# Optimization experiments

Measured on AMD Instinct MI355X. Metric: run time of the kernel, lower is better.

Reference implementation:

```python
import jax, jax.numpy as jnp
import numpy as np

B, T_TEXT, HID = 16, 512, 512
MAX_LEN = 2048
DP_CH, DP_K = 256, 3
PP_CH, PP_K, PP_LAYERS = 384, 5, 5
N_BINS = 256


def conv1d_same(x, w, b, pad):
    # x: [B, C_in, T], w: [C_out, C_in, K] -> [B, C_out, T]
    xp = jnp.pad(x, ((0, 0), (0, 0), (pad, pad)))
    y = jax.lax.conv_general_dilated(xp, w, (1,), 'VALID',
                                     dimension_numbers=('NCH', 'OIH', 'NCH'))
    return y + b[None, :, None]


def channel_ln(x, g, beta, eps=1e-5):
    # LayerNorm over channel dim of [B, C, T] (torch LayerNorm with dim=1)
    m = jnp.mean(x, axis=1, keepdims=True)
    v = jnp.mean((x - m) ** 2, axis=1, keepdims=True)
    return (x - m) / jnp.sqrt(v + eps) * g[None, :, None] + beta[None, :, None]


def sinusoidal_pos(T, dim):
    # fairseq-style sinusoidal embedding, positions start at padding_idx+1 = 1
    half = dim // 2
    inv = jnp.exp(jnp.arange(half, dtype=jnp.float32) * (-np.log(10000.0) / (half - 1)))
    pos = jnp.arange(1, T + 1, dtype=jnp.float32)
    ang = pos[:, None] * inv[None, :]
    return jnp.concatenate([jnp.sin(ang), jnp.cos(ang)], axis=1)  # [T, dim]


def setup_inputs() -> dict:
    key = jax.random.key(0)
    ks = jax.random.split(key, 16)
    sd = lambda fan: 1.0 / np.sqrt(fan)
    inp = {}
    inp['x'] = jax.random.normal(ks[0], (B, T_TEXT, HID), dtype=jnp.float32)
    inp['duration'] = jax.random.randint(ks[1], (B, T_TEXT), 0, 7, dtype=jnp.int32)
    inp['src_mask'] = jnp.zeros((B, T_TEXT), dtype=bool)
    inp['max_len'] = MAX_LEN
    # duration predictor params (2 conv layers + linear)
    inp['dp_w0'] = jax.random.normal(ks[2], (DP_CH, HID, DP_K)) * sd(HID * DP_K)
    inp['dp_w1'] = jax.random.normal(ks[3], (DP_CH, DP_CH, DP_K)) * sd(DP_CH * DP_K)
    inp['dp_b'] = jnp.zeros((2, DP_CH))
    inp['dp_g'] = jnp.ones((2, DP_CH))
    inp['dp_beta'] = jnp.zeros((2, DP_CH))
    inp['dp_lin_w'] = jax.random.normal(ks[4], (DP_CH, 1)) * sd(DP_CH)
    inp['dp_lin_b'] = jnp.zeros((1,))
    # pitch predictor params (5 conv layers + linear, odim=2 for use_uv)
    inp['pp_w0'] = jax.random.normal(ks[5], (PP_CH, HID, PP_K)) * sd(HID * PP_K)
    inp['pp_w_rest'] = jax.random.normal(ks[6], (PP_LAYERS - 1, PP_CH, PP_CH, PP_K)) * sd(PP_CH * PP_K)
    inp['pp_b'] = jnp.zeros((PP_LAYERS, PP_CH))
    inp['pp_g'] = jnp.ones((PP_LAYERS, PP_CH))
    inp['pp_beta'] = jnp.zeros((PP_LAYERS, PP_CH))
    inp['pp_lin_w'] = jax.random.normal(ks[7], (PP_CH, 2)) * sd(PP_CH)
    inp['pp_lin_b'] = jnp.zeros((2,))
    inp['pos_alpha'] = jnp.ones((1,))
    inp['pitch_emb'] = jax.random.normal(ks[8], (N_BINS, HID)) * 0.02
    inp['pitch_bins'] = jnp.linspace(-1.0, 1.0, N_BINS - 1)  # linear quantization, stats min/max
    return inp


def reference(x, duration, src_mask, max_len, dp_w0, dp_w1, dp_b, dp_g, dp_beta,
              dp_lin_w, dp_lin_b, pp_w0, pp_w_rest, pp_b, pp_g, pp_beta,
              pp_lin_w, pp_lin_b, pos_alpha, pitch_emb, pitch_bins):
    Bn, T, H = x.shape
    keep = 1.0 - src_mask.astype(x.dtype)  # [B,T], 1 where valid

    # ---- DurationPredictor (log-domain durations) ----
    h = jnp.transpose(x, (0, 2, 1))  # [B,H,T]
    for i, w in enumerate([dp_w0, dp_w1]):
        h = conv1d_same(h, w, dp_b[i], (DP_K - 1) // 2)
        h = jax.nn.relu(h)
        h = channel_ln(h, dp_g[i], dp_beta[i])
        h = h * keep[:, None, :]
    log_dur = (jnp.einsum('bct,co->bto', h, dp_lin_w) + dp_lin_b) * keep[:, :, None]
    log_dur = log_dur[..., 0]  # [B,T]

    # ---- LengthRegulator: vectorized variable-repeat via searchsorted ----
    cum = jnp.cumsum(duration, axis=1)  # [B,T]
    frames = jnp.arange(max_len)
    tok = jax.vmap(lambda c: jnp.searchsorted(c, frames, side='right'))(cum)  # [B,max_len]
    mel_len = cum[:, -1]
    fmask = (frames[None, :] < mel_len[:, None]).astype(x.dtype)  # [B,max_len]
    mel = jnp.take_along_axis(x, jnp.minimum(tok, T - 1)[..., None], axis=1) * fmask[..., None]

    # ---- VariancePredictor (pitch, odim=2 for f0 + uv) ----
    pe = sinusoidal_pos(max_len, H)  # [max_len, H]
    p = mel + pos_alpha[0] * pe[None]
    p = jnp.transpose(p, (0, 2, 1))  # [B,H,max_len]
    for i in range(PP_LAYERS):
        w = pp_w0 if i == 0 else pp_w_rest[i - 1]
        p = conv1d_same(p, w, pp_b[i], (PP_K - 1) // 2)
        p = jax.nn.relu(p)
        p = channel_ln(p, pp_g[i], pp_beta[i])
    pitch_pred = jnp.einsum('bct,co->bto', p, pp_lin_w) + pp_lin_b  # [B,max_len,2]

    # ---- bucketize f0 channel + embedding add ----
    idx = jnp.searchsorted(pitch_bins, pitch_pred[..., 0], side='left')  # torch.bucketize
    p_embed = pitch_emb[idx]  # [B,max_len,H]
    out = mel + p_embed
    return out, log_dur, pitch_pred, mel_len
```

## Files before the change

kernel.cpp:

```cpp
#include <hip/hip_runtime.h>
#include <cstdint>
#include <cstddef>

constexpr int BB      = 16;
constexpr int T_TEXT  = 512;
constexpr int HID     = 512;
constexpr int MAX_LEN = 2048;
constexpr int DP_CH   = 256;
constexpr int PP_CH   = 384;

typedef unsigned short u16;
typedef unsigned int   u32;
typedef short bf16x8 __attribute__((ext_vector_type(8)));
typedef float f32x4  __attribute__((ext_vector_type(4)));
typedef float f32x16 __attribute__((ext_vector_type(16)));

__device__ __forceinline__ void gload_lds16(const void* g, void* l) {
  __builtin_amdgcn_global_load_lds(
      (const __attribute__((address_space(1))) u32*)g,
      (__attribute__((address_space(3))) u32*)l, 16, 0, 0);
}

template <int N> __device__ __forceinline__ void vm_wait() {
  if constexpr (N == 0)      asm volatile("s_waitcnt vmcnt(0)" ::: "memory");
  else if constexpr (N == 3) asm volatile("s_waitcnt vmcnt(3)" ::: "memory");
  else if constexpr (N == 5) asm volatile("s_waitcnt vmcnt(5)" ::: "memory");
  else static_assert(N == 0, "unsupported vmcnt literal");
}

__device__ __forceinline__ u16 f2bf(float v) {
  union { float f; u32 u; } a;
  a.f = v;
  u32 r = (a.u + 0x7FFFu + ((a.u >> 16) & 1u)) >> 16;
  return (u16)r;
}
__device__ __forceinline__ float bf2f(u16 h) {
  union { u32 u; float f; } a;
  a.u = (u32)h << 16;
  return a.f;
}

__global__ __launch_bounds__(256) void pack_w_k(const float* __restrict__ w,
                                                u16* __restrict__ p,
                                                int O, int I, int KT) {
  int NF  = O >> 4, NCB = I >> 5;
  int total = KT * NCB * NF * 64;
  int idx = blockIdx.x * 256 + threadIdx.x;
  if (idx >= total) return;
  int l  = idx & 63;
  int f  = (idx >> 6) % NF;
  int cb = ((idx >> 6) / NF) % NCB;
  int k  = (idx >> 6) / (NF * NCB);
  int o  = f * 16 + (l & 15);
  int ib = cb * 32 + (l >> 4) * 8;
  u16* pd = p + ((size_t)((k * NCB + cb) * NF + f)) * 512 + (size_t)l * 8;
#pragma unroll
  for (int j = 0; j < 8; ++j)
    pd[j] = f2bf(w[((size_t)o * I + ib + j) * KT + k]);
}

__global__ __launch_bounds__(256) void pack_w32_k(const float* __restrict__ w,
                                                  u16* __restrict__ p,
                                                  int O, int I, int KT) {
  int G = O >> 5, NCB = I >> 5;
  int total = KT * NCB * G * 2 * 64;
  int idx = blockIdx.x * 256 + threadIdx.x;
  if (idx >= total) return;
  int l  = idx & 63;
  int ks = (idx >> 6) & 1;
  int g  = (idx >> 7) % G;
  int cb = ((idx >> 7) / G) % NCB;
  int k  = (idx >> 7) / (G * NCB);
  int o  = g * 32 + (l & 31);
  int ib = cb * 32 + ks * 16 + (l >> 5) * 8;
  u16* pd = p + (size_t)idx * 8;
#pragma unroll
  for (int j = 0; j < 8; ++j)
    pd[j] = f2bf(w[((size_t)o * I + ib + j) * KT + k]);
}

template <int CIN, int COUT, int KT, int MT, int WM, int WN, int OPAD, bool F32OUT>
__global__ __launch_bounds__(WM * WN * 64)
void gemm_conv_ln(const u16* __restrict__ a, const u16* __restrict__ wp,
                  const float* __restrict__ bias, const float* __restrict__ gamma,
                  const float* __restrict__ beta,
                  u16* __restrict__ o, float* __restrict__ fo, int T) {
  constexpr int WAVES   = WM * WN;
  constexpr int THREADS = WAVES * 64;
  constexpr int RS    = MT + KT - 1;
  constexpr int NCB   = CIN / 32;
  constexpr int NF    = COUT / 16;
  constexpr int Mfr   = MT / (16 * WM);
  constexpr int Nfr   = NF / WN;
  constexpr int A_ONE = RS * 64;
  constexpr int B_ONE = NF * 1024;
  constexpr int B_OFF = 2 * A_ONE;
  constexpr int RED_OFF = B_OFF + 2 * B_ONE;
  constexpr int CPW = 4 * RS / WAVES;

  const int TpIn  = T + KT - 1;
  const int TpOut = T + 2 * OPAD;

  const int tid  = threadIdx.x;
  const int wave = tid >> 6;
  const int lane = tid & 63;
  const int sl   = lane & 15;
  const int q    = lane >> 4;
  const int wm   = wave / WN;
  const int wn   = wave % WN;
  const int waveM0 = wm * Mfr * 16;
  const int f0   = wn * Nfr;
  const int t0   = blockIdx.x * MT;
  const int b    = blockIdx.y;

  extern __shared__ __align__(16) char smem[];
  const u16* abase_g = a + ((size_t)b * TpIn + t0) * CIN;

  auto stageA = [&](int buf, int cb) {
    char* lbase = smem + buf * A_ONE;
#pragma unroll
    for (int j = 0; j < CPW; j += 64) {
      int c   = wave * CPW + j + lane;
      int qc  = c / RS;
      int row = c - qc * RS;
      if (j + lane < CPW)
        gload_lds16(abase_g + (size_t)row * CIN + cb * 32 + qc * 8,
                    lbase + (size_t)(wave * CPW + j) * 16);
    }
  };
  auto stageB = [&](int buf, int k, int cb) {
    const u16* src = wp + ((size_t)(k * NCB + cb) * NF) * 512;
    char* lbase = smem + B_OFF + buf * B_ONE;
#pragma unroll
    for (int i = tid; i < NF * 64; i += THREADS) {
      gload_lds16(src + (size_t)i * 8, lbase + (size_t)(i - lane) * 16);
    }
  };

  f32x4 acc[Mfr][Nfr];
#pragma unroll
  for (int mf = 0; mf < Mfr; ++mf)
#pragma unroll
    for (int nf = 0; nf < Nfr; ++nf) acc[mf][nf] = (f32x4)0.f;

  stageA(0, 0);
  stageB(0, 0, 0);
  asm volatile("s_waitcnt vmcnt(0)" ::: "memory");
  __syncthreads();
  int ab = 0, bb = 0;
  for (int cb = 0; cb < NCB; ++cb) {
    for (int k = 0; k < KT; ++k) {
      if (k + 1 < KT) {
        stageB(bb ^ 1, k + 1, cb);
      } else if (cb + 1 < NCB) {
        stageB(bb ^ 1, 0, cb + 1);
        stageA(ab ^ 1, cb + 1);
      }
      bf16x8 A[Mfr], Bf[Nfr];
      const char* ab_l = smem + ab * A_ONE;
#pragma unroll
      for (int mf = 0; mf < Mfr; ++mf) {
        int row = waveM0 + mf * 16 + sl + k;
        A[mf] = *(const bf16x8*)(ab_l + (q * RS + row) * 16);
      }
      const char* bb_l = smem + B_OFF + bb * B_ONE;
#pragma unroll
      for (int nf = 0; nf < Nfr; ++nf)
        Bf[nf] = *(const bf16x8*)(bb_l + (size_t)(f0 + nf) * 1024 + lane * 16);
#pragma unroll
      for (int nf = 0; nf < Nfr; ++nf)
#pragma unroll
        for (int mf = 0; mf < Mfr; ++mf)
          acc[mf][nf] = __builtin_amdgcn_mfma_f32_16x16x32_bf16(
              A[mf], Bf[nf], acc[mf][nf], 0, 0, 0);
      asm volatile("s_waitcnt vmcnt(0)" ::: "memory");
      __syncthreads();
      bb ^= 1;
      if (k == KT - 1) ab ^= 1;
    }
  }

  float bc[Nfr], gc[Nfr], btc[Nfr];
#pragma unroll
  for (int nf = 0; nf < Nfr; ++nf) {
    int col = (f0 + nf) * 16 + sl;
    bc[nf]  = bias[col];
    gc[nf]  = gamma[col];
    btc[nf] = beta[col];
  }

  float* reds  = (float*)(smem + RED_OFF);
  float* redss = reds + MT * WN;

#pragma unroll
  for (int mf = 0; mf < Mfr; ++mf) {
#pragma unroll
    for (int r = 0; r < 4; ++r) {
      float s = 0.f, ss2 = 0.f;
#pragma unroll
      for (int nf = 0; nf < Nfr; ++nf) {
        float x = acc[mf][nf][r] + bc[nf];
        x = fmaxf(x, 0.f);
        acc[mf][nf][r] = x;
        s += x;
        ss2 = fmaf(x, x, ss2);
      }
#pragma unroll
      for (int off = 1; off < 16; off <<= 1) {
        s   += __shfl_xor(s, off, 64);
        ss2 += __shfl_xor(ss2, off, 64);
      }
      if (sl == 0) {
        int rowb = waveM0 + mf * 16 + q * 4 + r;
        reds[rowb * WN + wn]  = s;
        redss[rowb * WN + wn] = ss2;
      }
    }
  }
  __syncthreads();

#pragma unroll
  for (int mf = 0; mf < Mfr; ++mf) {
#pragma unroll
    for (int r = 0; r < 4; ++r) {
      int rowb = waveM0 + mf * 16 + q * 4 + r;
      float s = 0.f, ss2 = 0.f;
#pragma unroll
      for (int w2 = 0; w2 < WN; ++w2) {
        s   += reds[rowb * WN + w2];
        ss2 += redss[rowb * WN + w2];
      }
      float mean = s * (1.f / COUT);
      float var  = ss2 * (1.f / COUT) - mean * mean;
      float rstd = 1.f / sqrtf(var + 1e-5f);
      int trow = t0 + rowb;
#pragma unroll
      for (int nf = 0; nf < Nfr; ++nf) {
        int col = (f0 + nf) * 16 + sl;
        float y = (acc[mf][nf][r] - mean) * rstd * gc[nf] + btc[nf];
        if constexpr (F32OUT) {
          fo[((size_t)b * T + trow) * COUT + col] = y;
        } else {
          o[((size_t)b * TpOut + OPAD + trow) * COUT + col] = f2bf(y);
        }
      }
    }
  }

  if constexpr (!F32OUT && OPAD > 0) {
    if (blockIdx.x == 0) {
      for (int i = tid; i < OPAD * COUT; i += THREADS) {
        o[(size_t)b * TpOut * COUT + i] = 0;
        o[((size_t)b * TpOut + OPAD + T) * COUT + i] = 0;
      }
    }
  }
}

constexpr int gemm_lds(int MT, int KT, int COUT, int WN_) {
  return 2 * (MT + KT - 1) * 64 + 2 * (COUT / 16) * 1024 + MT * WN_ * 8;
}

template <int CIN, int COUT, int KT, int MT, int WM, int WN, int OPAD>
__global__ __launch_bounds__(WM * WN * 64)
void gemm_conv_ln32(const u16* __restrict__ a, const u16* __restrict__ wp,
                    const float* __restrict__ bias, const float* __restrict__ gamma,
                    const float* __restrict__ beta,
                    u16* __restrict__ o, int T) {
  constexpr int WAVES   = WM * WN;
  constexpr int THREADS = WAVES * 64;
  constexpr int RS    = MT + KT - 1;
  constexpr int NCB   = CIN / 32;
  constexpr int G     = COUT / 32;
  constexpr int Mfr   = MT / (32 * WM);
  constexpr int Nfr   = G / WN;
  constexpr int A_ONE = RS * 64;
  constexpr int NFB   = G * 2;
  constexpr int B_ONE = NFB * 1024;
  constexpr int B_OFF = 2 * A_ONE;
  constexpr int RED_OFF = B_OFF + KT * B_ONE;
  constexpr int NSTEPS = NCB * KT;
  static_assert((4 * RS) % WAVES == 0, "A chunks split evenly per wave");
  static_assert((NFB * 64) % THREADS == 0, "B chunks split evenly");
  constexpr int CPW = 4 * RS / WAVES;

  const int TpIn  = T + KT - 1;
  const int TpOut = T + 2 * OPAD;

  const int tid  = threadIdx.x;
  const int wave = tid >> 6;
  const int lane = tid & 63;
  const int l31  = lane & 31;
  const int lh   = lane >> 5;
  const int wm   = wave / WN;
  const int wn   = wave % WN;
  const int waveM0 = wm * Mfr * 32;
  const int g0   = wn * Nfr;
  const int t0   = blockIdx.x * MT;
  const int b    = blockIdx.y;

  extern __shared__ __align__(16) char smem[];
  const u16* abase_g = a + ((size_t)b * TpIn + t0) * CIN;

  auto stageA = [&](int buf, int cb) {
    char* lbase = smem + buf * A_ONE;
#pragma unroll
    for (int j = 0; j < CPW; j += 64) {
      int c   = wave * CPW + j + lane;
      int qc  = c / RS;
      int row = c - qc * RS;
      if (j + lane < CPW)
        gload_lds16(abase_g + (size_t)row * CIN + cb * 32 + qc * 8,
                    lbase + (size_t)(wave * CPW + j) * 16);
    }
  };
  auto stageB = [&](int buf, int k, int cb) {
    const u16* src = wp + ((size_t)(k * NCB + cb) * NFB) * 512;
    char* lbase = smem + B_OFF + buf * B_ONE;
#pragma unroll
    for (int i = tid; i < NFB * 64; i += THREADS) {
      gload_lds16(src + (size_t)i * 8, lbase + (size_t)(i - lane) * 16);
    }
  };

  f32x16 acc[Mfr][Nfr];
#pragma unroll
  for (int mf = 0; mf < Mfr; ++mf)
#pragma unroll
    for (int nf = 0; nf < Nfr; ++nf) acc[mf][nf] = (f32x16)0.f;

  stageA(0, 0);
  stageB(0, 0, 0);
  stageB(1, 1, 0);
  vm_wait<3>();
  __builtin_amdgcn_s_barrier();

  for (int cb = 0; cb < NCB; ++cb) {
    const char* ab_l = smem + (cb & 1) * A_ONE;
#pragma unroll
    for (int j = 0; j < KT; ++j) {
      const int s = cb * KT + j;
      __builtin_amdgcn_sched_barrier(0);

      bf16x8 A[Mfr][2], Bf[Nfr][2];
      const char* bb_l = smem + B_OFF + j * B_ONE;
#pragma unroll
      for (int mf = 0; mf < Mfr; ++mf) {
        int row = waveM0 + mf * 32 + l31 + j;
#pragma unroll
        for (int ks = 0; ks < 2; ++ks)
          A[mf][ks] = *(const bf16x8*)(ab_l + ((ks * 2 + lh) * RS + row) * 16);
      }
#pragma unroll
      for (int nf = 0; nf < Nfr; ++nf)
#pragma unroll
        for (int ks = 0; ks < 2; ++ks)
          Bf[nf][ks] = *(const bf16x8*)(bb_l + ((size_t)((g0 + nf) * 2 + ks)) * 1024 + lane * 16);

      const bool boundary = (j == 0 && cb + 1 < NCB);
      if (boundary) stageA((cb + 1) & 1, cb + 1);
      if (s + 2 < NSTEPS) {
        const int s2 = s + 2;
        stageB(s2 % KT, s2 % KT, s2 / KT);
      }

      __builtin_amdgcn_s_setprio(1);
#pragma unroll
      for (int ks = 0; ks < 2; ++ks)
#pragma unroll
        for (int nf = 0; nf < Nfr; ++nf)
#pragma unroll
          for (int mf = 0; mf < Mfr; ++mf)
            acc[mf][nf] = __builtin_amdgcn_mfma_f32_32x32x16_bf16(
                A[mf][ks], Bf[nf][ks], acc[mf][nf], 0, 0, 0);
      __builtin_amdgcn_s_setprio(0);

      __builtin_amdgcn_sched_barrier(0);
      if (s + 2 < NSTEPS) {
        if (boundary) vm_wait<5>();
        else          vm_wait<3>();
      } else {
        vm_wait<0>();
      }
      __builtin_amdgcn_s_barrier();
    }
  }

  float bc[Nfr], gc[Nfr], btc[Nfr];
#pragma unroll
  for (int nf = 0; nf < Nfr; ++nf) {
    int col = (g0 + nf) * 32 + l31;
    bc[nf]  = bias[col];
    gc[nf]  = gamma[col];
    btc[nf] = beta[col];
  }

  float* reds  = (float*)(smem + RED_OFF);
  float* redss = reds + MT * WN;
  float* mrs   = redss + MT * WN;

#pragma unroll
  for (int mf = 0; mf < Mfr; ++mf) {
#pragma unroll
    for (int r = 0; r < 16; ++r) {
      float s = 0.f, ss2 = 0.f;
#pragma unroll
      for (int nf = 0; nf < Nfr; ++nf) {
        float x = acc[mf][nf][r] + bc[nf];
        x = fmaxf(x, 0.f);
        acc[mf][nf][r] = x;
        s += x;
        ss2 = fmaf(x, x, ss2);
      }
#pragma unroll
      for (int off = 1; off < 32; off <<= 1) {
        s   += __shfl_xor(s, off, 64);
        ss2 += __shfl_xor(ss2, off, 64);
      }
      if (l31 == 0) {
        int row = waveM0 + mf * 32 + (r & 3) + 8 * (r >> 2) + 4 * lh;
        reds[row * WN + wn]  = s;
        redss[row * WN + wn] = ss2;
      }
    }
  }
  __syncthreads();

  if (tid < MT) {
    float s = 0.f, ss2 = 0.f;
#pragma unroll
    for (int w2 = 0; w2 < WN; ++w2) {
      s   += reds[tid * WN + w2];
      ss2 += redss[tid * WN + w2];
    }
    float mean = s * (1.f / COUT);
    float var  = ss2 * (1.f / COUT) - mean * mean;
    mrs[tid * 2]     = mean;
    mrs[tid * 2 + 1] = 1.f / sqrtf(var + 1e-5f);
  }
  __syncthreads();

#pragma unroll
  for (int mf = 0; mf < Mfr; ++mf) {
#pragma unroll
    for (int r = 0; r < 16; ++r) {
      int row = waveM0 + mf * 32 + (r & 3) + 8 * (r >> 2) + 4 * lh;
      float mean = mrs[row * 2];
      float rstd = mrs[row * 2 + 1];
      int trow = t0 + row;
#pragma unroll
      for (int nf = 0; nf < Nfr; ++nf) {
        int col = (g0 + nf) * 32 + l31;
        float y = (acc[mf][nf][r] - mean) * rstd * gc[nf] + btc[nf];
        o[((size_t)b * TpOut + OPAD + trow) * COUT + col] = f2bf(y);
      }
    }
  }

  if constexpr (OPAD > 0) {
    if (blockIdx.x == 0) {
      for (int i = tid; i < OPAD * COUT; i += THREADS) {
        o[(size_t)b * TpOut * COUT + i] = 0;
        o[((size_t)b * TpOut + OPAD + T) * COUT + i] = 0;
      }
    }
  }
}

constexpr int gemm_lds32(int MT, int KT, int COUT, int WN_) {
  return 2 * (MT + KT - 1) * 64 + KT * (COUT / 32) * 2 * 1024 +
         MT * WN_ * 8 + MT * 8;
}

__global__ __launch_bounds__(256) void split_x_k(const float* __restrict__ x,
                                                 u16* __restrict__ xb) {
  int b = blockIdx.y;
  int row = blockIdx.x * 4 + (threadIdx.x >> 6);
  int lane = threadIdx.x & 63;
  if (row >= T_TEXT + 2) return;
  size_t out = ((size_t)b * (T_TEXT + 2) + row) * HID;
  if (row == 0 || row == T_TEXT + 1) {
    for (int h = lane; h < HID; h += 64) xb[out + h] = 0;
    return;
  }
  const float* xr = x + ((size_t)b * T_TEXT + row - 1) * HID;
  for (int h = lane; h < HID; h += 64) xb[out + h] = f2bf(xr[h]);
}

__global__ __launch_bounds__(256) void dp_head_k(const float* __restrict__ h,
                                                 const float* __restrict__ w,
                                                 const float* __restrict__ b,
                                                 float* __restrict__ out) {
  int tid = threadIdx.x;
  int wv = tid >> 6, lane = tid & 63;
  int row = blockIdx.x * 4 + wv;
  const float* hr = h + (size_t)row * DP_CH;
  float s = 0.f;
  for (int c = lane; c < DP_CH; c += 64) s = fmaf(hr[c], w[c], s);
#pragma unroll
  for (int off = 1; off < 64; off <<= 1) s += __shfl_xor(s, off, 64);
  if (lane == 0) out[row] = s + b[0];
}

__global__ __launch_bounds__(512) void cumsum_k(const int* __restrict__ dur,
                                                int* __restrict__ cum,
                                                float* __restrict__ mel_len_out) {
  __shared__ int s[T_TEXT];
  int b = blockIdx.x, t = threadIdx.x;
  s[t] = dur[b * T_TEXT + t];
  __syncthreads();
  for (int off = 1; off < T_TEXT; off <<= 1) {
    int add = (t >= off) ? s[t - off] : 0;
    __syncthreads();
    s[t] += add;
    __syncthreads();
  }
  cum[b * T_TEXT + t] = s[t];
  if (t == T_TEXT - 1) mel_len_out[b] = (float)s[t];
}

__global__ __launch_bounds__(256) void pe_k(float* __restrict__ pe) {
  int f = blockIdx.x * 4 + (threadIdx.x >> 6);
  int lane = threadIdx.x & 63;
  float posf = (float)(f + 1);
  const float kfac = -0.03611898185f;
  float* pr = pe + (size_t)f * HID;
  for (int h = lane; h < HID / 2; h += 64) {
    float inv = expf((float)h * kfac);
    float ang = posf * inv;
    float sv, cv;
    sincosf(ang, &sv, &cv);
    pr[h]           = sv;
    pr[h + HID / 2] = cv;
  }
}

__global__ __launch_bounds__(256) void build_p_k(const float* __restrict__ x,
                                                 const int* __restrict__ cum,
                                                 const float* __restrict__ alpha_p,
                                                 const float* __restrict__ pe,
                                                 u16* __restrict__ pb) {
  __shared__ int cs[T_TEXT];
  int b = blockIdx.y, tid = threadIdx.x;
  for (int i = tid; i < T_TEXT; i += 256) cs[i] = cum[b * T_TEXT + i];
  __syncthreads();
  int row = blockIdx.x * 4 + (tid >> 6);
  int lane = tid & 63;
  if (row >= MAX_LEN + 4) return;
  size_t out = ((size_t)b * (MAX_LEN + 4) + row) * HID;
  if (row < 2 || row >= MAX_LEN + 2) {
    for (int h = lane; h < HID; h += 64) pb[out + h] = 0;
    return;
  }
  int f = row - 2;
  int lo = 0, hi = T_TEXT;
  while (lo < hi) {
    int mid = (lo + hi) >> 1;
    if (cs[mid] <= f) lo = mid + 1; else hi = mid;
  }
  int src = min(lo, T_TEXT - 1);
  float fm = (f < cs[T_TEXT - 1]) ? 1.f : 0.f;
  float alpha = alpha_p[0];
  const float* xr = x + ((size_t)b * T_TEXT + src) * HID;
  const float* pr = pe + (size_t)f * HID;
  for (int h = lane; h < HID; h += 64)
    pb[out + h] = f2bf(fmaf(alpha, pr[h], xr[h] * fm));
}

__global__ __launch_bounds__(256) void final_head_k(
    const u16* __restrict__ p, const float* __restrict__ x,
    const int* __restrict__ cum, const float* __restrict__ lw,
    const float* __restrict__ lb, const float* __restrict__ bins,
    const float* __restrict__ emb, float* __restrict__ out0,
    float* __restrict__ pred) {
  __shared__ int cs[T_TEXT];
  int b = blockIdx.y, tid = threadIdx.x;
  for (int i = tid; i < T_TEXT; i += 256) cs[i] = cum[b * T_TEXT + i];
  __syncthreads();
  int wv = tid >> 6, lane = tid & 63;
  int f = blockIdx.x * 4 + wv;
  size_t row = (size_t)b * MAX_LEN + f;
  const u16* prr = p + row * PP_CH;
  float s0 = 0.f, s1 = 0.f;
  for (int c = lane; c < PP_CH; c += 64) {
    float v = bf2f(prr[c]);
    s0 = fmaf(v, lw[2 * c], s0);
    s1 = fmaf(v, lw[2 * c + 1], s1);
  }
#pragma unroll
  for (int off = 1; off < 64; off <<= 1) {
    s0 += __shfl_xor(s0, off, 64);
    s1 += __shfl_xor(s1, off, 64);
  }
  float p0 = s0 + lb[0];
  float p1 = s1 + lb[1];
  if (lane == 0) {
    pred[row * 2] = p0;
    pred[row * 2 + 1] = p1;
  }
  int lo = 0, hi = 255;
  while (lo < hi) {
    int mid = (lo + hi) >> 1;
    if (bins[mid] < p0) lo = mid + 1; else hi = mid;
  }
  int lo2 = 0, hi2 = T_TEXT;
  while (lo2 < hi2) {
    int mid = (lo2 + hi2) >> 1;
    if (cs[mid] <= f) lo2 = mid + 1; else hi2 = mid;
  }
  int src = min(lo2, T_TEXT - 1);
  float fm = (f < cs[T_TEXT - 1]) ? 1.f : 0.f;
  const float* xr = x + ((size_t)b * T_TEXT + src) * HID;
  const float* er = emb + (size_t)lo * HID;
  float* orow = out0 + row * HID;
  for (int h = lane; h < HID; h += 64) orow[h] = fmaf(xr[h], fm, er[h]);
}

extern "C" void kernel_launch(void* const* d_in, const int* in_sizes, int n_in,
                              void* d_out, int out_size, void* d_ws,
                              size_t ws_size, hipStream_t stream) {
  (void)in_sizes; (void)n_in; (void)out_size; (void)ws_size;

  const float* x          = (const float*)d_in[0];
  const int*   duration   = (const int*)d_in[1];
  const float* dp_w0      = (const float*)d_in[4];
  const float* dp_w1      = (const float*)d_in[5];
  const float* dp_b       = (const float*)d_in[6];
  const float* dp_g       = (const float*)d_in[7];
  const float* dp_beta    = (const float*)d_in[8];
  const float* dp_lin_w   = (const float*)d_in[9];
  const float* dp_lin_b   = (const float*)d_in[10];
  const float* pp_w0      = (const float*)d_in[11];
  const float* pp_w_rest  = (const float*)d_in[12];
  const float* pp_b       = (const float*)d_in[13];
  const float* pp_g       = (const float*)d_in[14];
  const float* pp_beta    = (const float*)d_in[15];
  const float* pp_lin_w   = (const float*)d_in[16];
  const float* pp_lin_b   = (const float*)d_in[17];
  const float* pos_alpha  = (const float*)d_in[18];
  const float* pitch_emb  = (const float*)d_in[19];
  const float* pitch_bins = (const float*)d_in[20];

  char* w8 = (char*)d_ws;
  size_t off = 0;
  auto alloc = [&](size_t bytes) {
    char* pp = w8 + off;
    off += (bytes + 255) & ~(size_t)255;
    return pp;
  };
  u16*   xb    = (u16*)alloc((size_t)BB * 514 * 512 * 2);
  u16*   dp1   = (u16*)alloc((size_t)BB * 514 * 256 * 2);
  float* dp2   = (float*)alloc((size_t)BB * 512 * 256 * 4);
  u16*   Pb    = (u16*)alloc((size_t)BB * 2052 * 512 * 2);
  u16*   ppA   = (u16*)alloc((size_t)BB * 2052 * 384 * 2);
  u16*   ppB   = (u16*)alloc((size_t)BB * 2052 * 384 * 2);
  u16*   pfin  = (u16*)alloc((size_t)BB * 2048 * 384 * 2);
  float* peT   = (float*)alloc((size_t)MAX_LEN * HID * 4);
  u16*   pwdp0 = (u16*)alloc((size_t)3 * 512 * 256 * 2);
  u16*   pwdp1 = (u16*)alloc((size_t)3 * 256 * 256 * 2);
  u16*   pwpp0 = (u16*)alloc((size_t)5 * 512 * 384 * 2);
  u16*   pwppr = (u16*)alloc((size_t)4 * 5 * 384 * 384 * 2);
  int*   cum   = (int*)alloc((size_t)BB * T_TEXT * 4);

  float* out0       = (float*)d_out;
  float* log_dur    = out0 + (size_t)BB * MAX_LEN * HID;
  float* pitch_pred = log_dur + (size_t)BB * T_TEXT;
  float* mel_len    = pitch_pred + (size_t)BB * MAX_LEN * 2;

  pack_w_k<<<dim3((3 * (512/32) * (256/16) * 64 + 255) / 256), dim3(256), 0, stream>>>(
      dp_w0, pwdp0, 256, 512, 3);
  pack_w_k<<<dim3((3 * (256/32) * (256/16) * 64 + 255) / 256), dim3(256), 0, stream>>>(
      dp_w1, pwdp1, 256, 256, 3);
  pack_w32_k<<<dim3((5 * 16 * 12 * 2 * 64 + 255) / 256), dim3(256), 0, stream>>>(
      pp_w0, pwpp0, 384, 512, 5);
  for (int l = 0; l < 4; ++l)
    pack_w32_k<<<dim3((5 * 12 * 12 * 2 * 64 + 255) / 256), dim3(256), 0, stream>>>(
        pp_w_rest + (size_t)l * 384 * 384 * 5,
        pwppr + (size_t)l * (5 * 384 * 384), 384, 384, 5);

  split_x_k<<<dim3(129, BB), dim3(256), 0, stream>>>(x, xb);
  cumsum_k<<<dim3(BB), dim3(512), 0, stream>>>(duration, cum, mel_len);
  pe_k<<<dim3(MAX_LEN / 4), dim3(256), 0, stream>>>(peT);

  constexpr int LDS_DP = gemm_lds(64, 3, 256, 2);
  gemm_conv_ln<512, 256, 3, 64, 2, 2, 1, false>
      <<<dim3(8, BB), dim3(256), LDS_DP, stream>>>(
          xb, pwdp0, dp_b, dp_g, dp_beta, dp1, nullptr, T_TEXT);
  gemm_conv_ln<256, 256, 3, 64, 2, 2, 1, true>
      <<<dim3(8, BB), dim3(256), LDS_DP, stream>>>(
          dp1, pwdp1, dp_b + 256, dp_g + 256, dp_beta + 256,
          nullptr, dp2, T_TEXT);
  dp_head_k<<<dim3(BB * T_TEXT / 4), dim3(256), 0, stream>>>(dp2, dp_lin_w,
                                                             dp_lin_b, log_dur);

  build_p_k<<<dim3(513, BB), dim3(256), 0, stream>>>(x, cum, pos_alpha, peT, Pb);

  constexpr int LDS_PP = gemm_lds32(128, 5, 384, 4);
  gemm_conv_ln32<512, 384, 5, 128, 2, 4, 2>
      <<<dim3(16, BB), dim3(512), LDS_PP, stream>>>(
          Pb, pwpp0, pp_b, pp_g, pp_beta, ppA, MAX_LEN);
  gemm_conv_ln32<384, 384, 5, 128, 2, 4, 2>
      <<<dim3(16, BB), dim3(512), LDS_PP, stream>>>(
          ppA, pwppr + 0 * (5 * 384 * 384),
          pp_b + 384, pp_g + 384, pp_beta + 384, ppB, MAX_LEN);
  gemm_conv_ln32<384, 384, 5, 128, 2, 4, 2>
      <<<dim3(16, BB), dim3(512), LDS_PP, stream>>>(
          ppB, pwppr + 1 * (5 * 384 * 384),
          pp_b + 768, pp_g + 768, pp_beta + 768, ppA, MAX_LEN);
  gemm_conv_ln32<384, 384, 5, 128, 2, 4, 2>
      <<<dim3(16, BB), dim3(512), LDS_PP, stream>>>(
          ppA, pwppr + 2 * (5 * 384 * 384),
          pp_b + 1152, pp_g + 1152, pp_beta + 1152, ppB, MAX_LEN);
  gemm_conv_ln32<384, 384, 5, 128, 2, 4, 0>
      <<<dim3(16, BB), dim3(512), LDS_PP, stream>>>(
          ppB, pwppr + 3 * (5 * 384 * 384),
          pp_b + 1536, pp_g + 1536, pp_beta + 1536, pfin, MAX_LEN);

  final_head_k<<<dim3(MAX_LEN / 4, BB), dim3(256), 0, stream>>>(
      pfin, x, cum, pp_lin_w, pp_lin_b, pitch_bins, pitch_emb, out0, pitch_pred);
}
```

Measured before the change: 453.7 us.

## Switch pitch conv GEMMs to 16x16 MFMA with 64-wide K blocks

Replaces the 32x32x16 MFMA pitch-predictor conv kernel with a 16x16x32 variant that stages 64 input channels per step. Weights are packed in the 16-wide layout shared with the duration predictor, so the separate 32-wide packer is dropped. The three-stage B prefetch ring becomes a double buffer with waits before the compute. The separate mean/rstd pass is folded into each thread's epilogue, which removes one barrier. The schedule no longer overlaps loads with the MFMAs, and the different fragment shape and LDS footprint may lower MFMA efficiency.

```diff
diff --git a/kernel.cpp b/kernel.cpp
--- a/kernel.cpp
+++ b/kernel.cpp
@@ -13,7 +13,6 @@
 typedef unsigned int   u32;
 typedef short bf16x8 __attribute__((ext_vector_type(8)));
 typedef float f32x4  __attribute__((ext_vector_type(4)));
-typedef float f32x16 __attribute__((ext_vector_type(16)));
 
 __device__ __forceinline__ void gload_lds16(const void* g, void* l) {
   __builtin_amdgcn_global_load_lds(
@@ -23,8 +22,8 @@
 
 template <int N> __device__ __forceinline__ void vm_wait() {
   if constexpr (N == 0)      asm volatile("s_waitcnt vmcnt(0)" ::: "memory");
-  else if constexpr (N == 3) asm volatile("s_waitcnt vmcnt(3)" ::: "memory");
-  else if constexpr (N == 5) asm volatile("s_waitcnt vmcnt(5)" ::: "memory");
+  else if constexpr (N == 6) asm volatile("s_waitcnt vmcnt(6)" ::: "memory");
+  else if constexpr (N == 9) asm volatile("s_waitcnt vmcnt(9)" ::: "memory");
   else static_assert(N == 0, "unsupported vmcnt literal");
 }
 
@@ -54,26 +53,6 @@
   int o  = f * 16 + (l & 15);
   int ib = cb * 32 + (l >> 4) * 8;
   u16* pd = p + ((size_t)((k * NCB + cb) * NF + f)) * 512 + (size_t)l * 8;
-#pragma unroll
-  for (int j = 0; j < 8; ++j)
-    pd[j] = f2bf(w[((size_t)o * I + ib + j) * KT + k]);
-}
-
-__global__ __launch_bounds__(256) void pack_w32_k(const float* __restrict__ w,
-                                                  u16* __restrict__ p,
-                                                  int O, int I, int KT) {
-  int G = O >> 5, NCB = I >> 5;
-  int total = KT * NCB * G * 2 * 64;
-  int idx = blockIdx.x * 256 + threadIdx.x;
-  if (idx >= total) return;
-  int l  = idx & 63;
-  int ks = (idx >> 6) & 1;
-  int g  = (idx >> 7) % G;
-  int cb = ((idx >> 7) / G) % NCB;
-  int k  = (idx >> 7) / (G * NCB);
-  int o  = g * 32 + (l & 31);
-  int ib = cb * 32 + ks * 16 + (l >> 5) * 8;
-  u16* pd = p + (size_t)idx * 8;
 #pragma unroll
   for (int j = 0; j < 8; ++j)
     pd[j] = f2bf(w[((size_t)o * I + ib + j) * KT + k]);
@@ -131,7 +110,6 @@
   auto stageB = [&](int buf, int k, int cb) {
     const u16* src = wp + ((size_t)(k * NCB + cb) * NF) * 512;
     char* lbase = smem + B_OFF + buf * B_ONE;
-#pragma unroll
     for (int i = tid; i < NF * 64; i += THREADS) {
       gload_lds16(src + (size_t)i * 8, lbase + (size_t)(i - lane) * 16);
     }
@@ -263,26 +241,29 @@
 
 template <int CIN, int COUT, int KT, int MT, int WM, int WN, int OPAD>
 __global__ __launch_bounds__(WM * WN * 64)
-void gemm_conv_ln32(const u16* __restrict__ a, const u16* __restrict__ wp,
+void gemm_conv_ln64(const u16* __restrict__ a, const u16* __restrict__ wp,
                     const float* __restrict__ bias, const float* __restrict__ gamma,
                     const float* __restrict__ beta,
                     u16* __restrict__ o, int T) {
   constexpr int WAVES   = WM * WN;
   constexpr int THREADS = WAVES * 64;
-  constexpr int RS    = MT + KT - 1;
-  constexpr int NCB   = CIN / 32;
-  constexpr int G     = COUT / 32;
-  constexpr int Mfr   = MT / (32 * WM);
-  constexpr int Nfr   = G / WN;
-  constexpr int A_ONE = RS * 64;
-  constexpr int NFB   = G * 2;
-  constexpr int B_ONE = NFB * 1024;
-  constexpr int B_OFF = 2 * A_ONE;
-  constexpr int RED_OFF = B_OFF + KT * B_ONE;
-  constexpr int NSTEPS = NCB * KT;
-  static_assert((4 * RS) % WAVES == 0, "A chunks split evenly per wave");
-  static_assert((NFB * 64) % THREADS == 0, "B chunks split evenly");
-  constexpr int CPW = 4 * RS / WAVES;
+  constexpr int RS     = MT + KT - 1;
+  constexpr int NCB    = CIN / 64;
+  constexpr int NCB32  = CIN / 32;
+  constexpr int NF     = COUT / 16;
+  constexpr int Mfr    = MT / (16 * WM);
+  constexpr int Nfr    = NF / WN;
+  constexpr int A_ONE  = RS * 128;
+  constexpr int B_ONE  = 2 * NF * 1024;
+  constexpr int B_OFF  = 2 * A_ONE;
+  constexpr int RED_OFF = B_OFF + 2 * B_ONE;
+  static_assert(CIN % 64 == 0, "BK=64 needs CIN multiple of 64");
+  static_assert((8 * RS) % WAVES == 0, "A chunks split evenly per wave");
+  static_assert((2 * NF * 64) % THREADS == 0, "B chunks split evenly");
+  constexpr int CPW     = 8 * RS / WAVES;
+  constexpr int A_INSTS = (CPW + 63) / 64;
+  constexpr int VMB     = (2 * NF * 64) / THREADS;
+  constexpr int VMBA    = VMB + A_INSTS;
 
   const int TpIn  = T + KT - 1;
   const int TpOut = T + 2 * OPAD;
@@ -290,12 +271,12 @@
   const int tid  = threadIdx.x;
   const int wave = tid >> 6;
   const int lane = tid & 63;
-  const int l31  = lane & 31;
-  const int lh   = lane >> 5;
+  const int sl   = lane & 15;
+  const int q    = lane >> 4;
   const int wm   = wave / WN;
   const int wn   = wave % WN;
-  const int waveM0 = wm * Mfr * 32;
-  const int g0   = wn * Nfr;
+  const int waveM0 = wm * Mfr * 16;
+  const int f0   = wn * Nfr;
   const int t0   = blockIdx.x * MT;
   const int b    = blockIdx.y;
 
@@ -310,59 +291,59 @@
       int qc  = c / RS;
       int row = c - qc * RS;
       if (j + lane < CPW)
-        gload_lds16(abase_g + (size_t)row * CIN + cb * 32 + qc * 8,
+        gload_lds16(abase_g + (size_t)row * CIN + cb * 64 + qc * 8,
                     lbase + (size_t)(wave * CPW + j) * 16);
     }
   };
   auto stageB = [&](int buf, int k, int cb) {
-    const u16* src = wp + ((size_t)(k * NCB + cb) * NFB) * 512;
+    const u16* src = wp + ((size_t)(k * NCB32 + 2 * cb) * NF) * 512;
     char* lbase = smem + B_OFF + buf * B_ONE;
 #pragma unroll
-    for (int i = tid; i < NFB * 64; i += THREADS) {
+    for (int i = tid; i < 2 * NF * 64; i += THREADS) {
       gload_lds16(src + (size_t)i * 8, lbase + (size_t)(i - lane) * 16);
     }
   };
 
-  f32x16 acc[Mfr][Nfr];
+  f32x4 acc[Mfr][Nfr];
 #pragma unroll
   for (int mf = 0; mf < Mfr; ++mf)
 #pragma unroll
-    for (int nf = 0; nf < Nfr; ++nf) acc[mf][nf] = (f32x16)0.f;
+    for (int nf = 0; nf < Nfr; ++nf) acc[mf][nf] = (f32x4)0.f;
 
   stageA(0, 0);
   stageB(0, 0, 0);
-  stageB(1, 1, 0);
-  vm_wait<3>();
-  __builtin_amdgcn_s_barrier();
-
+
+  int ab = 0, bb = 0;
   for (int cb = 0; cb < NCB; ++cb) {
-    const char* ab_l = smem + (cb & 1) * A_ONE;
-#pragma unroll
-    for (int j = 0; j < KT; ++j) {
-      const int s = cb * KT + j;
+    for (int k = 0; k < KT; ++k) {
+      if (k + 1 < KT) {
+        stageB(bb ^ 1, k + 1, cb);
+        vm_wait<VMB>();
+      } else if (cb + 1 < NCB) {
+        stageB(bb ^ 1, 0, cb + 1);
+        stageA(ab ^ 1, cb + 1);
+        vm_wait<VMBA>();
+      } else {
+        vm_wait<0>();
+      }
+      __builtin_amdgcn_s_barrier();
       __builtin_amdgcn_sched_barrier(0);
 
       bf16x8 A[Mfr][2], Bf[Nfr][2];
-      const char* bb_l = smem + B_OFF + j * B_ONE;
+      const char* ab_l = smem + ab * A_ONE;
+      const char* bb_l = smem + B_OFF + bb * B_ONE;
 #pragma unroll
       for (int mf = 0; mf < Mfr; ++mf) {
-        int row = waveM0 + mf * 32 + l31 + j;
+        int row = waveM0 + mf * 16 + sl + k;
 #pragma unroll
         for (int ks = 0; ks < 2; ++ks)
-          A[mf][ks] = *(const bf16x8*)(ab_l + ((ks * 2 + lh) * RS + row) * 16);
+          A[mf][ks] = *(const bf16x8*)(ab_l + ((ks * 4 + q) * RS + row) * 16);
       }
 #pragma unroll
       for (int nf = 0; nf < Nfr; ++nf)
 #pragma unroll
         for (int ks = 0; ks < 2; ++ks)
-          Bf[nf][ks] = *(const bf16x8*)(bb_l + ((size_t)((g0 + nf) * 2 + ks)) * 1024 + lane * 16);
-
-      const bool boundary = (j == 0 && cb + 1 < NCB);
-      if (boundary) stageA((cb + 1) & 1, cb + 1);
-      if (s + 2 < NSTEPS) {
-        const int s2 = s + 2;
-        stageB(s2 % KT, s2 % KT, s2 / KT);
-      }
+          Bf[nf][ks] = *(const bf16x8*)(bb_l + (size_t)(ks * NF + f0 + nf) * 1024 + lane * 16);
 
       __builtin_amdgcn_s_setprio(1);
 #pragma unroll
@@ -371,25 +352,21 @@
         for (int nf = 0; nf < Nfr; ++nf)
 #pragma unroll
           for (int mf = 0; mf < Mfr; ++mf)
-            acc[mf][nf] = __builtin_amdgcn_mfma_f32_32x32x16_bf16(
+            acc[mf][nf] = __builtin_amdgcn_mfma_f32_16x16x32_bf16(
                 A[mf][ks], Bf[nf][ks], acc[mf][nf], 0, 0, 0);
       __builtin_amdgcn_s_setprio(0);
 
       __builtin_amdgcn_sched_barrier(0);
-      if (s + 2 < NSTEPS) {
-        if (boundary) vm_wait<5>();
-        else          vm_wait<3>();
-      } else {
-        vm_wait<0>();
-      }
       __builtin_amdgcn_s_barrier();
+      bb ^= 1;
+      if (k == KT - 1) ab ^= 1;
     }
   }
 
   float bc[Nfr], gc[Nfr], btc[Nfr];
 #pragma unroll
   for (int nf = 0; nf < Nfr; ++nf) {
-    int col = (g0 + nf) * 32 + l31;
+    int col = (f0 + nf) * 16 + sl;
     bc[nf]  = bias[col];
     gc[nf]  = gamma[col];
     btc[nf] = beta[col];
@@ -397,12 +374,11 @@
 
   float* reds  = (float*)(smem + RED_OFF);
   float* redss = reds + MT * WN;
-  float* mrs   = redss + MT * WN;
 
 #pragma unroll
   for (int mf = 0; mf < Mfr; ++mf) {
 #pragma unroll
-    for (int r = 0; r < 16; ++r) {
+    for (int r = 0; r < 4; ++r) {
       float s = 0.f, ss2 = 0.f;
 #pragma unroll
       for (int nf = 0; nf < Nfr; ++nf) {
@@ -413,44 +389,37 @@
         ss2 = fmaf(x, x, ss2);
       }
 #pragma unroll
-      for (int off = 1; off < 32; off <<= 1) {
+      for (int off = 1; off < 16; off <<= 1) {
         s   += __shfl_xor(s, off, 64);
         ss2 += __shfl_xor(ss2, off, 64);
       }
-      if (l31 == 0) {
-        int row = waveM0 + mf * 32 + (r & 3) + 8 * (r >> 2) + 4 * lh;
-        reds[row * WN + wn]  = s;
-        redss[row * WN + wn] = ss2;
+      if (sl == 0) {
+        int rowb = waveM0 + mf * 16 + q * 4 + r;
+        reds[rowb * WN + wn]  = s;
+        redss[rowb * WN + wn] = ss2;
       }
     }
   }
   __syncthreads();
 
-  if (tid < MT) {
-    float s = 0.f, ss2 = 0.f;
-#pragma unroll
-    for (int w2 = 0; w2 < WN; ++w2) {
-      s   += reds[tid * WN + w2];
-      ss2 += redss[tid * WN + w2];
-    }
-    float mean = s * (1.f / COUT);
-    float var  = ss2 * (1.f / COUT) - mean * mean;
-    mrs[tid * 2]     = mean;
-    mrs[tid * 2 + 1] = 1.f / sqrtf(var + 1e-5f);
-  }
-  __syncthreads();
-
 #pragma unroll
   for (int mf = 0; mf < Mfr; ++mf) {
 #pragma unroll
-    for (int r = 0; r < 16; ++r) {
-      int row = waveM0 + mf * 32 + (r & 3) + 8 * (r >> 2) + 4 * lh;
-      float mean = mrs[row * 2];
-      float rstd = mrs[row * 2 + 1];
-      int trow = t0 + row;
+    for (int r = 0; r < 4; ++r) {
+      int rowb = waveM0 + mf * 16 + q * 4 + r;
+      float s = 0.f, ss2 = 0.f;
+#pragma unroll
+      for (int w2 = 0; w2 < WN; ++w2) {
+        s   += reds[rowb * WN + w2];
+        ss2 += redss[rowb * WN + w2];
+      }
+      float mean = s * (1.f / COUT);
+      float var  = ss2 * (1.f / COUT) - mean * mean;
+      float rstd = 1.f / sqrtf(var + 1e-5f);
+      int trow = t0 + rowb;
 #pragma unroll
       for (int nf = 0; nf < Nfr; ++nf) {
-        int col = (g0 + nf) * 32 + l31;
+        int col = (f0 + nf) * 16 + sl;
         float y = (acc[mf][nf][r] - mean) * rstd * gc[nf] + btc[nf];
         o[((size_t)b * TpOut + OPAD + trow) * COUT + col] = f2bf(y);
       }
@@ -467,9 +436,8 @@
   }
 }
 
-constexpr int gemm_lds32(int MT, int KT, int COUT, int WN_) {
-  return 2 * (MT + KT - 1) * 64 + KT * (COUT / 32) * 2 * 1024 +
-         MT * WN_ * 8 + MT * 8;
+constexpr int gemm_lds64(int MT, int KT, int COUT, int WN_) {
+  return 2 * (MT + KT - 1) * 128 + 2 * (COUT / 16) * 2048 + MT * WN_ * 8;
 }
 
 __global__ __launch_bounds__(256) void split_x_k(const float* __restrict__ x,
@@ -667,16 +635,16 @@
   float* pitch_pred = log_dur + (size_t)BB * T_TEXT;
   float* mel_len    = pitch_pred + (size_t)BB * MAX_LEN * 2;
 
-  pack_w_k<<<dim3((3 * (512/32) * (256/16) * 64 + 255) / 256), dim3(256), 0, stream>>>(
-      dp_w0, pwdp0, 256, 512, 3);
-  pack_w_k<<<dim3((3 * (256/32) * (256/16) * 64 + 255) / 256), dim3(256), 0, stream>>>(
-      dp_w1, pwdp1, 256, 256, 3);
-  pack_w32_k<<<dim3((5 * 16 * 12 * 2 * 64 + 255) / 256), dim3(256), 0, stream>>>(
-      pp_w0, pwpp0, 384, 512, 5);
+  auto pk = [&](const float* src, u16* dst, int O, int I, int KT) {
+    int tot = KT * (I / 32) * (O / 16) * 64;
+    pack_w_k<<<dim3((tot + 255) / 256), dim3(256), 0, stream>>>(src, dst, O, I, KT);
+  };
+  pk(dp_w0, pwdp0, 256, 512, 3);
+  pk(dp_w1, pwdp1, 256, 256, 3);
+  pk(pp_w0, pwpp0, 384, 512, 5);
   for (int l = 0; l < 4; ++l)
-    pack_w32_k<<<dim3((5 * 12 * 12 * 2 * 64 + 255) / 256), dim3(256), 0, stream>>>(
-        pp_w_rest + (size_t)l * 384 * 384 * 5,
-        pwppr + (size_t)l * (5 * 384 * 384), 384, 384, 5);
+    pk(pp_w_rest + (size_t)l * 384 * 384 * 5,
+       pwppr + (size_t)l * (5 * 384 * 384), 384, 384, 5);
 
   split_x_k<<<dim3(129, BB), dim3(256), 0, stream>>>(x, xb);
   cumsum_k<<<dim3(BB), dim3(512), 0, stream>>>(duration, cum, mel_len);
@@ -695,23 +663,23 @@
 
   build_p_k<<<dim3(513, BB), dim3(256), 0, stream>>>(x, cum, pos_alpha, peT, Pb);
 
-  constexpr int LDS_PP = gemm_lds32(128, 5, 384, 4);
-  gemm_conv_ln32<512, 384, 5, 128, 2, 4, 2>
+  constexpr int LDS_PP = gemm_lds64(128, 5, 384, 4);
+  gemm_conv_ln64<512, 384, 5, 128, 2, 4, 2>
       <<<dim3(16, BB), dim3(512), LDS_PP, stream>>>(
           Pb, pwpp0, pp_b, pp_g, pp_beta, ppA, MAX_LEN);
-  gemm_conv_ln32<384, 384, 5, 128, 2, 4, 2>
+  gemm_conv_ln64<384, 384, 5, 128, 2, 4, 2>
       <<<dim3(16, BB), dim3(512), LDS_PP, stream>>>(
           ppA, pwppr + 0 * (5 * 384 * 384),
           pp_b + 384, pp_g + 384, pp_beta + 384, ppB, MAX_LEN);
-  gemm_conv_ln32<384, 384, 5, 128, 2, 4, 2>
+  gemm_conv_ln64<384, 384, 5, 128, 2, 4, 2>
       <<<dim3(16, BB), dim3(512), LDS_PP, stream>>>(
           ppB, pwppr + 1 * (5 * 384 * 384),
           pp_b + 768, pp_g + 768, pp_beta + 768, ppA, MAX_LEN);
-  gemm_conv_ln32<384, 384, 5, 128, 2, 4, 2>
+  gemm_conv_ln64<384, 384, 5, 128, 2, 4, 2>
       <<<dim3(16, BB), dim3(512), LDS_PP, stream>>>(
           ppA, pwppr + 2 * (5 * 384 * 384),
           pp_b + 1152, pp_g + 1152, pp_beta + 1152, ppB, MAX_LEN);
-  gemm_conv_ln32<384, 384, 5, 128, 2, 4, 0>
+  gemm_conv_ln64<384, 384, 5, 128, 2, 4, 0>
       <<<dim3(16, BB), dim3(512), LDS_PP, stream>>>(
           ppB, pwppr + 3 * (5 * 384 * 384),
           pp_b + 1536, pp_g + 1536, pp_beta + 1536, pfin, MAX_LEN);
```

New measurement: 574.9 us. 1.27x slower.
